# Kernel optimization log

Hardware: AMD Instinct MI355X
Metric: run time of the kernel (lower is better)

The kernel has to match this reference:

```python
import jax, jax.numpy as jnp
import numpy as np
import math

B, T, C, NH, LEVEL = 2, 2048, 1024, 16, 3


def _build_sets(T, level):
    # hierarchical dyadic sets: levels `level`..floor(log2(T)), step 2^l
    sets = []
    levelmax = int(math.floor(math.log2(T)))
    for l in range(level, levelmax + 1):
        step = 2 ** l
        for i in range(T // step):
            sets.append((i * step, (i + 1) * step - 1))
    b = np.asarray(sets, dtype=np.int32)
    return b[:, 0], b[:, 1]


def setup_inputs() -> dict:
    key = jax.random.key(0)
    kx, kw1, kw2 = jax.random.split(key, 3)
    x = jax.random.normal(kx, (B, T, C), dtype=jnp.float32)
    # torch nn.Linear stores weight as (out_features, in_features); y = x @ W.T
    W_attn = jax.random.normal(kw1, (3 * C, C), dtype=jnp.float32) * (C ** -0.5)
    W_proj = jax.random.normal(kw2, (C, C), dtype=jnp.float32) * (C ** -0.5)
    return {"x": x, "W_attn": W_attn, "W_proj": W_proj}


def _get_slice(xc, l_idx, r_idx):
    # xc: (B,NH,T,hs) cumulative sums; returns sum over [l_idx, r_idx]
    r = xc[:, :, r_idx, :]
    l = xc[:, :, l_idx - 1, :] * (l_idx >= 1)[None, None, :, None].astype(xc.dtype)
    return r - l


def _forward(x, W_attn, W_proj):
    hs = C // NH
    scale = hs ** -0.5
    qkv = x @ W_attn.T                      # (B,T,3C)
    q, k, v = jnp.split(qkv, 3, axis=2)
    heads = lambda t: t.reshape(B, T, NH, hs).transpose(0, 2, 1, 3)  # (B,NH,T,hs)
    q, k, v = heads(q), heads(k), heads(v)
    phi = lambda t: jax.nn.elu(t) + 1.0     # feature_map = 'elu_plus'
    q_phi, k_phi = phi(q), phi(k)
    k_cum = jnp.cumsum(k_phi, axis=2)
    v_cum = jnp.cumsum(v, axis=2)

    l_np, r_np = _build_sets(T, LEVEL)
    l_idx, r_idx = jnp.asarray(l_np), jnp.asarray(r_np)
    K = _get_slice(k_cum, l_idx, r_idx)     # (B,NH,S,hs)
    V = _get_slice(v_cum, l_idx, r_idx)

    t_idx = jnp.arange(T)
    mask = t_idx[:, None] >= r_idx[None, :]                 # (T,S)
    logits = jnp.einsum('bhtd,bhsd->bhts', q, K) * scale    # raw q here (as in source)
    logits = jnp.where(mask[None, None], logits, -jnp.inf)

    # tail term over last (t mod 2^level)+1 tokens, uses q_phi
    Lmin = 2 ** LEVEL
    tail_len = t_idx % Lmin + 1
    l_tail = t_idx - tail_len + 1
    K_tail = _get_slice(k_cum, l_tail, t_idx)               # (B,NH,T,hs)
    V_tail = _get_slice(v_cum, l_tail, t_idx)
    tail_logit = jnp.sum(q_phi * K_tail, axis=-1) * scale   # (B,NH,T)

    full = jnp.concatenate([logits, tail_logit[..., None]], axis=-1)
    att = jax.nn.softmax(full, axis=-1)
    out = jnp.einsum('bhts,bhsd->bhtd', att[..., :-1], V) + att[..., -1:] * V_tail
    out = out.transpose(0, 2, 1, 3).reshape(B, T, C)
    return out @ W_proj.T


def reference(x, W_attn, W_proj):
    return _forward(x, W_attn, W_proj)
```

## Files before the change

### kernel.cpp

```cpp
#include <hip/hip_runtime.h>
#include <hip/hip_bf16.h>
#include <stdint.h>

#define B_    2
#define T_    2048
#define CD    1024
#define NH_   16
#define HS_   64
#define NSETS 511
#define NSP   512
#define QKV_LD 3072
#define NEGBIG (-3.4e38f)

typedef __attribute__((ext_vector_type(8))) short  short8;
typedef __attribute__((ext_vector_type(4))) float  f32x4;

__device__ __forceinline__ unsigned short f2bf(float f) {
  unsigned u = __float_as_uint(f);
  unsigned r = 0x7FFFu + ((u >> 16) & 1u);
  return (unsigned short)((u + r) >> 16);
}
__device__ __forceinline__ float bf2f(unsigned short h) {
  return __uint_as_float(((unsigned)h) << 16);
}
__device__ __forceinline__ float elu1(float x) {
  return x > 0.f ? x + 1.f : __expf(x);
}
__device__ __forceinline__ void gload16(const unsigned short* g, short* l) {
  __builtin_amdgcn_global_load_lds(
      (const __attribute__((address_space(1))) unsigned int*)g,
      (__attribute__((address_space(3))) unsigned int*)l, 16, 0, 0);
}

__global__ __launch_bounds__(256) void split3_kernel(
    const float* __restrict__ x, const float* __restrict__ Wa,
    const float* __restrict__ Wp,
    unsigned short* __restrict__ xh, unsigned short* __restrict__ xl,
    unsigned short* __restrict__ wah, unsigned short* __restrict__ wal,
    unsigned short* __restrict__ wph) {
  int bid = blockIdx.x;
  const float* src; unsigned short *hi, *lo; int base;
  if (bid < 16384)      { src = x;  hi = xh;  lo = xl;  base = bid; }
  else if (bid < 24576) { src = Wa; hi = wah; lo = wal; base = bid - 16384; }
  else if (bid < 28672) { src = Wa; hi = wah; lo = nullptr; base = bid - 16384; }
  else                  { src = Wp; hi = wph; lo = nullptr; base = bid - 28672; }
  int i = base * 256 + threadIdx.x;
  float v = src[i];
  unsigned short h = f2bf(v);
  hi[i] = h;
  if (lo) lo[i] = f2bf(v - bf2f(h));
}

template<int SPLIT>
__device__ __forceinline__ void gemm_body(
    short* lds,
    const unsigned short* __restrict__ Ah, const unsigned short* __restrict__ Al,
    const unsigned short* __restrict__ Bh, const unsigned short* __restrict__ Bl,
    float* __restrict__ Cmat, int K, int ldc, int row0, int col0)
{
  const int tid  = threadIdx.x;
  const int lane = tid & 63;
  const int w    = tid >> 6;
  const int wr   = w >> 1, wc = w & 1;

  f32x4 acc[4][4];
  #pragma unroll
  for (int a = 0; a < 4; ++a)
    #pragma unroll
    for (int b = 0; b < 4; ++b)
      acc[a][b] = (f32x4){0.f, 0.f, 0.f, 0.f};

  const int rlane = lane & 15;
  const int kgrp  = lane >> 4;
  const int rsw   = (kgrp ^ (rlane & 3) ^ ((rlane >> 2) & 3)) << 4;

  const int slr = lane >> 2;
  const int sch = (lane & 3) ^ (slr & 3) ^ ((slr >> 2) & 3);

  const unsigned short* ssrc;
  size_t srb;
  short* sbase;
  if (SPLIT) {
    ssrc = (w == 0) ? Ah : (w == 1) ? Bh : (w == 2) ? Al : Bl;
    srb  = (w & 1) ? (size_t)col0 : (size_t)row0;
    sbase = &lds[w * 4096];
  } else {
    ssrc = (w & 1) ? Bh : Ah;
    srb  = (w & 1) ? (size_t)col0 : (size_t)row0;
    sbase = &lds[(w & 1) * 4096 + (w >> 1) * 2048];
    srb += (size_t)(w >> 1) * 64;
  }

  for (int kt = 0; kt < K; kt += 32) {
    __syncthreads();
    const unsigned short* g0 = ssrc + (srb + slr) * K + kt + (sch << 3);
    if (SPLIT) {
      #pragma unroll
      for (int i = 0; i < 8; ++i)
        gload16(g0 + (size_t)i * 16 * K, sbase + i * 512);
    } else {
      #pragma unroll
      for (int i = 0; i < 4; ++i)
        gload16(g0 + (size_t)i * 16 * K, sbase + i * 512);
    }
    __syncthreads();

    short8 aH[4], bH[4], aL[4], bL[4];
    #pragma unroll
    for (int m = 0; m < 4; ++m) {
      int r    = wr * 64 + m * 16 + rlane;
      int cidx = wc * 64 + m * 16 + rlane;
      aH[m] = *(const short8*)((const char*)lds + r * 64 + rsw);
      bH[m] = *(const short8*)((const char*)lds + 8192 + cidx * 64 + rsw);
      if (SPLIT) {
        aL[m] = *(const short8*)((const char*)lds + 16384 + r * 64 + rsw);
        bL[m] = *(const short8*)((const char*)lds + 24576 + cidx * 64 + rsw);
      }
    }
    #pragma unroll
    for (int mm = 0; mm < 4; ++mm)
      #pragma unroll
      for (int nn = 0; nn < 4; ++nn) {
        acc[mm][nn] = __builtin_amdgcn_mfma_f32_16x16x32_bf16(aH[mm], bH[nn], acc[mm][nn], 0, 0, 0);
        if (SPLIT) {
          acc[mm][nn] = __builtin_amdgcn_mfma_f32_16x16x32_bf16(aH[mm], bL[nn], acc[mm][nn], 0, 0, 0);
          acc[mm][nn] = __builtin_amdgcn_mfma_f32_16x16x32_bf16(aL[mm], bH[nn], acc[mm][nn], 0, 0, 0);
        }
      }
  }

  const int rl = (lane >> 4) * 4;
  const int cl = lane & 15;
  #pragma unroll
  for (int mm = 0; mm < 4; ++mm)
    #pragma unroll
    for (int nn = 0; nn < 4; ++nn)
      #pragma unroll
      for (int r = 0; r < 4; ++r) {
        int row = row0 + wr * 64 + mm * 16 + rl + r;
        int col = col0 + wc * 64 + nn * 16 + cl;
        Cmat[(size_t)row * ldc + col] = acc[mm][nn][r];
      }
}

__global__ __launch_bounds__(256) void gemm_qkv(
    const unsigned short* __restrict__ xh, const unsigned short* __restrict__ xl,
    const unsigned short* __restrict__ wah, const unsigned short* __restrict__ wal,
    float* __restrict__ qkv)
{
  __shared__ short lds[4 * 4096];
  int bid = blockIdx.x;
  if (bid < 512) {
    int swb = (bid & 7) * 64 + (bid >> 3);
    int bx = swb & 15, by = swb >> 4;
    gemm_body<1>(lds, xh, xl, wah, wal, qkv,
                 CD, QKV_LD, by * 128, bx * 128);
  } else {
    int p = bid - 512;
    int swb = (p & 7) * 32 + (p >> 3);
    int bx = swb & 7, by = swb >> 3;
    gemm_body<0>(lds, xh, nullptr, wah + (size_t)2048 * CD, nullptr,
                 qkv + 2048, CD, QKV_LD, by * 128, bx * 128);
  }
}

template<int SPLIT>
__global__ __launch_bounds__(256) void gemm_bt(
    const unsigned short* __restrict__ Ah, const unsigned short* __restrict__ Al,
    const unsigned short* __restrict__ Bh, const unsigned short* __restrict__ Bl,
    float* __restrict__ Cmat, int M, int N, int K, int ldc)
{
  constexpr int NT = SPLIT ? 4 : 2;
  __shared__ short lds[NT * 4096];
  const int nwg = gridDim.x;
  const int cpx = nwg >> 3;
  const int bid = blockIdx.x;
  const int swb = (bid & 7) * cpx + (bid >> 3);
  const int nbx = N >> 7;
  const int bx = swb % nbx;
  const int by = swb / nbx;
  gemm_body<SPLIT>(lds, Ah, Al, Bh, Bl, Cmat, K, ldc, by * 128, bx * 128);
}

__global__ __launch_bounds__(256) void cs_part(const float* __restrict__ qkv,
                                               float* __restrict__ part) {
  int blk = blockIdx.x;
  int q   = blk & 1;
  int seg = (blk >> 1) & 63;
  int b   = blk >> 7;
  int c   = threadIdx.x * 4;
  const float* src = qkv + (size_t)(b * T_ + seg * 32) * QKV_LD + CD + q * CD + c;
  float4 s = {0.f, 0.f, 0.f, 0.f};
  #pragma unroll 4
  for (int j = 0; j < 32; ++j) {
    float4 v = *(const float4*)(src + (size_t)j * QKV_LD);
    if (q == 0) {
      s.x += elu1(v.x); s.y += elu1(v.y); s.z += elu1(v.z); s.w += elu1(v.w);
    } else {
      s.x += v.x; s.y += v.y; s.z += v.z; s.w += v.w;
    }
  }
  *(float4*)(part + ((size_t)(b * 64 + seg) * 2048) + q * 1024 + c) = s;
}

__global__ void cs_prefix(float* __restrict__ part) {
  int idx = blockIdx.x * 256 + threadIdx.x;
  int b  = idx >> 11;
  int cc = idx & 2047;
  float v[64];
  #pragma unroll
  for (int s = 0; s < 64; ++s) v[s] = part[(size_t)(b * 64 + s) * 2048 + cc];
  float run = 0.f;
  #pragma unroll
  for (int s = 0; s < 64; ++s) { float t = v[s]; v[s] = run; run += t; }
  #pragma unroll
  for (int s = 0; s < 64; ++s) part[(size_t)(b * 64 + s) * 2048 + cc] = v[s];
}

__global__ __launch_bounds__(256) void cs_final(const float* __restrict__ qkv,
                                                const float* __restrict__ part,
                                                float* __restrict__ kcum,
                                                float* __restrict__ vcum) {
  int blk = blockIdx.x;
  int q   = blk & 1;
  int seg = (blk >> 1) & 63;
  int b   = blk >> 7;
  int c   = threadIdx.x * 4;
  int h   = c >> 6, d = c & 63;
  const float* src = qkv + (size_t)(b * T_ + seg * 32) * QKV_LD + CD + q * CD + c;
  float* dst = (q == 0 ? kcum : vcum) + ((size_t)(b * NH_ + h) * T_ + seg * 32) * HS_ + d;
  float4 s = *(const float4*)(part + ((size_t)(b * 64 + seg) * 2048) + q * 1024 + c);
  #pragma unroll 4
  for (int j = 0; j < 32; ++j) {
    float4 v = *(const float4*)(src + (size_t)j * QKV_LD);
    if (q == 0) {
      s.x += elu1(v.x); s.y += elu1(v.y); s.z += elu1(v.z); s.w += elu1(v.w);
    } else {
      s.x += v.x; s.y += v.y; s.z += v.z; s.w += v.w;
    }
    *(float4*)(dst + (size_t)j * HS_) = s;
  }
}

__global__ void build_sets(const float* __restrict__ kcum, const float* __restrict__ vcum,
                           unsigned short* __restrict__ Ksh, unsigned short* __restrict__ Ksl,
                           float* __restrict__ Vs, int* __restrict__ r_srt) {
  int idx = blockIdx.x * 256 + threadIdx.x;
  if (idx >= B_ * NH_ * NSP * HS_) return;
  int d  = idx & 63;
  int s  = (idx >> 6) & (NSP - 1);
  int bh = idx >> (6 + 9);
  if (s == NSETS) {
    size_t o = ((size_t)(bh << 9) + s) * HS_ + d;
    Ksh[o] = 0; Ksl[o] = 0; Vs[o] = 0.f;
    if (bh == 0 && d == 0) r_srt[s] = 0x7fffffff;
    return;
  }
  int lvl = 3, base = 0;
  while (s >= base + (T_ >> lvl)) { base += T_ >> lvl; ++lvl; }
  int i  = s - base;
  int m  = (i + 1) << lvl;
  int r  = m - 1;
  int li = i << lvl;
  int rank = lvl - 3;
  #pragma unroll
  for (int j = 3; j <= 11; ++j) rank += (m - 8) >> j;

  size_t rowr = ((size_t)bh * T_ + r) * HS_ + d;
  float kr = kcum[rowr], vr = vcum[rowr];
  if (li > 0) {
    size_t rowl = ((size_t)bh * T_ + li - 1) * HS_ + d;
    kr -= kcum[rowl];
    vr -= vcum[rowl];
  }
  size_t o = ((size_t)(bh << 9) + rank) * HS_ + d;
  unsigned short kh = f2bf(kr);
  Ksh[o] = kh;
  Ksl[o] = f2bf(kr - bf2f(kh));
  Vs[o]  = vr;
  if (bh == 0 && d == 0) r_srt[rank] = r;
}

__global__ __launch_bounds__(256) void vst_transpose(
    const float* __restrict__ Vs, unsigned short* __restrict__ Vst) {
  __shared__ float tile[64][65];
  int bh = blockIdx.x >> 3;
  int s0 = (blockIdx.x & 7) * 64;
  int tid = threadIdx.x;
  int srow = tid >> 2, c0 = (tid & 3) * 16;
  const float* src = Vs + ((size_t)(bh << 9) + s0 + srow) * HS_ + c0;
  #pragma unroll
  for (int j = 0; j < 4; ++j) {
    float4 v = *(const float4*)(src + j * 4);
    tile[srow][c0 + j*4 + 0] = v.x; tile[srow][c0 + j*4 + 1] = v.y;
    tile[srow][c0 + j*4 + 2] = v.z; tile[srow][c0 + j*4 + 3] = v.w;
  }
  __syncthreads();
  int d = tid >> 2, sq = (tid & 3) * 16;
  short8 a, b;
  #pragma unroll
  for (int j = 0; j < 8; ++j) {
    a[j] = (short)f2bf(tile[sq + j][d]);
    b[j] = (short)f2bf(tile[sq + 8 + j][d]);
  }
  unsigned short* dst = Vst + ((size_t)(bh << 6) + d) * NSP + s0 + sq;
  *(short8*)dst = a;
  *(short8*)(dst + 8) = b;
}

__global__ __launch_bounds__(256) void attn_mfma(
    const float* __restrict__ qkv, const float* __restrict__ kcum,
    const float* __restrict__ vcum,
    const unsigned short* __restrict__ Ksh, const unsigned short* __restrict__ Ksl,
    const unsigned short* __restrict__ Vst, const int* __restrict__ r_srt,
    unsigned short* __restrict__ attnb)
{
  __shared__ short Pl[4 * 2048];
  __shared__ short KV[3 * 4096];
  __shared__ int   rs_lds[NSP];

  const int blk = blockIdx.x;
  const int xcd = blk & 7;
  const int j   = blk >> 3;
  const int bhx = j >> 4;
  const int bh  = xcd * 4 + bhx;
  const int rb  = ((j & 15) + bhx * 4) & 15;
  const int b = bh >> 4, h = bh & 15;
  const int t0 = rb * 128;
  const int tid = threadIdx.x;
  const int lane = tid & 63;
  const int w = tid >> 6;
  const int col = lane & 15;
  const int kgrp = (lane >> 4) * 8;
  const float scale = 0.125f;

  const int srow = lane >> 3;
  const int scsw = ((lane & 7) ^ srow) * 8;

  auto stage_tile = [&](int s0) {
    #pragma unroll
    for (int L = w * 6; L < w * 6 + 6; ++L) {
      int a = L >> 3, i = L & 7;
      const unsigned short* src;
      if (a == 0)      src = Ksh + ((size_t)(bh << 9) + s0 + i * 8 + srow) * 64 + scsw;
      else if (a == 1) src = Ksl + ((size_t)(bh << 9) + s0 + i * 8 + srow) * 64 + scsw;
      else             src = Vst + ((size_t)(bh << 6) + i * 8 + srow) * NSP + s0 + scsw;
      gload16(src, KV + a * 4096 + i * 512 + lane * 8);
    }
  };

  short8 qh[2][2], ql[2][2];
  #pragma unroll
  for (int rr = 0; rr < 2; ++rr) {
    int qrow = t0 + w * 32 + rr * 16 + col;
    const float* qr = qkv + (size_t)(b * T_ + qrow) * QKV_LD + h * HS_;
    #pragma unroll
    for (int ks = 0; ks < 2; ++ks) {
      float4 v0 = *(const float4*)(qr + kgrp + ks * 32);
      float4 v1 = *(const float4*)(qr + kgrp + ks * 32 + 4);
      float vv[8] = {v0.x, v0.y, v0.z, v0.w, v1.x, v1.y, v1.z, v1.w};
      #pragma unroll
      for (int jj = 0; jj < 8; ++jj) {
        unsigned short hi = f2bf(vv[jj]);
        qh[rr][ks][jj] = (short)hi;
        ql[rr][ks][jj] = (short)f2bf(vv[jj] - bf2f(hi));
      }
    }
  }
  for (int s = tid; s < NSP; s += 256) rs_lds[s] = r_srt[s];

  int rows[2][4];
  #pragma unroll
  for (int rr = 0; rr < 2; ++rr)
    #pragma unroll
    for (int r = 0; r < 4; ++r)
      rows[rr][r] = t0 + w * 32 + rr * 16 + (lane >> 4) * 4 + r;

  f32x4 O[2][4];
  float mrun[2][4], lsum[2][4];
  #pragma unroll
  for (int rr = 0; rr < 2; ++rr)
    #pragma unroll
    for (int f = 0; f < 4; ++f) {
      O[rr][f] = (f32x4){0.f, 0.f, 0.f, 0.f};
      mrun[rr][f] = NEGBIG; lsum[rr][f] = 0.f;
    }

  int nmax = 0;
  #pragma unroll
  for (int jj = 3; jj <= 11; ++jj) nmax += (t0 + 128) >> jj;
  const int ntiles = (nmax + 63) >> 6;

  for (int tile = 0; tile < ntiles; ++tile) {
    const int s0 = tile * 64;
    stage_tile(s0);
    __syncthreads();

    f32x4 S[2][4];
    #pragma unroll
    for (int rr = 0; rr < 2; ++rr)
      #pragma unroll
      for (int f = 0; f < 4; ++f) S[rr][f] = (f32x4){0.f, 0.f, 0.f, 0.f};

    #pragma unroll
    for (int ks = 0; ks < 2; ++ks) {
      int chnk = (lane >> 4) + ks * 4;
      #pragma unroll
      for (int f = 0; f < 4; ++f) {
        int so = f * 16 + col;
        int kb = so * 128 + ((chnk ^ (so & 7)) << 4);
        short8 bHv = *(const short8*)((const char*)KV + kb);
        short8 bLv = *(const short8*)((const char*)KV + 8192 + kb);
        #pragma unroll
        for (int rr = 0; rr < 2; ++rr) {
          S[rr][f] = __builtin_amdgcn_mfma_f32_16x16x32_bf16(qh[rr][ks], bHv, S[rr][f], 0, 0, 0);
          S[rr][f] = __builtin_amdgcn_mfma_f32_16x16x32_bf16(qh[rr][ks], bLv, S[rr][f], 0, 0, 0);
          S[rr][f] = __builtin_amdgcn_mfma_f32_16x16x32_bf16(ql[rr][ks], bHv, S[rr][f], 0, 0, 0);
        }
      }
    }

    int rsv[4];
    #pragma unroll
    for (int f = 0; f < 4; ++f) rsv[f] = rs_lds[s0 + f * 16 + col];

    #pragma unroll
    for (int rr = 0; rr < 2; ++rr)
      #pragma unroll
      for (int f = 0; f < 4; ++f)
        #pragma unroll
        for (int r = 0; r < 4; ++r)
          S[rr][f][r] = (rsv[f] > rows[rr][r]) ? NEGBIG : S[rr][f][r] * scale;

    float mx[2][4];
    int pred = 1;
    #pragma unroll
    for (int rr = 0; rr < 2; ++rr)
      #pragma unroll
      for (int r = 0; r < 4; ++r) {
        mx[rr][r] = fmaxf(fmaxf(S[rr][0][r], S[rr][1][r]),
                          fmaxf(S[rr][2][r], S[rr][3][r]));
        pred &= (mx[rr][r] <= mrun[rr][r] + 8.f);
      }
    if (!__all(pred)) {
      #pragma unroll
      for (int rr = 0; rr < 2; ++rr)
        #pragma unroll
        for (int r = 0; r < 4; ++r) {
          float mt = mx[rr][r];
          mt = fmaxf(mt, __shfl_xor(mt, 1));
          mt = fmaxf(mt, __shfl_xor(mt, 2));
          mt = fmaxf(mt, __shfl_xor(mt, 4));
          mt = fmaxf(mt, __shfl_xor(mt, 8));
          float mv = fmaxf(mrun[rr][r], mt);
          float fs = __expf(mrun[rr][r] - mv);
          lsum[rr][r] *= fs;
          #pragma unroll
          for (int f = 0; f < 4; ++f) O[rr][f][r] *= fs;
          mrun[rr][r] = mv;
        }
    }

    char* pw = (char*)Pl + w * 4096;
    #pragma unroll
    for (int rr = 0; rr < 2; ++rr)
      #pragma unroll
      for (int r = 0; r < 4; ++r) {
        int rowr = rr * 16 + (lane >> 4) * 4 + r;
        int rswz = (rowr & 7) << 4;
        #pragma unroll
        for (int f = 0; f < 4; ++f) {
          float p = __expf(S[rr][f][r] - mrun[rr][r]);
          p = (rsv[f] > rows[rr][r]) ? 0.f : p;
          lsum[rr][r] += p;
          int addr = (rowr * 128 + (f * 16 + col) * 2) ^ rswz;
          *(unsigned short*)(pw + addr) = f2bf(p);
        }
      }

    #pragma unroll
    for (int ks = 0; ks < 2; ++ks) {
      int chnk = (lane >> 4) + ks * 4;
      int pb0 = (col * 128 + (kgrp + ks * 32) * 2) ^ ((col & 7) << 4);
      short8 pa0 = *(const short8*)(pw + pb0);
      short8 pa1 = *(const short8*)(pw + 2048 + pb0);
      #pragma unroll
      for (int f = 0; f < 4; ++f) {
        int dr = f * 16 + col;
        short8 bv = *(const short8*)((const char*)KV + 16384 + dr * 128 + ((chnk ^ (dr & 7)) << 4));
        O[0][f] = __builtin_amdgcn_mfma_f32_16x16x32_bf16(pa0, bv, O[0][f], 0, 0, 0);
        O[1][f] = __builtin_amdgcn_mfma_f32_16x16x32_bf16(pa1, bv, O[1][f], 0, 0, 0);
      }
    }

    __syncthreads();
  }

  float lrun[2][4];
  #pragma unroll
  for (int rr = 0; rr < 2; ++rr)
    #pragma unroll
    for (int r = 0; r < 4; ++r) {
      float l = lsum[rr][r];
      l += __shfl_xor(l, 1);
      l += __shfl_xor(l, 2);
      l += __shfl_xor(l, 4);
      l += __shfl_xor(l, 8);
      lrun[rr][r] = l;
    }

  float ztail[2];
  #pragma unroll
  for (int rr = 0; rr < 2; ++rr) {
    int trow = lane >> 2;
    int t = t0 + w * 32 + rr * 16 + trow;
    int d0 = (lane & 3) * 16;
    const float* qr = qkv + (size_t)(b * T_ + t) * QKV_LD + h * HS_ + d0;
    float qv[16];
    #pragma unroll
    for (int jj = 0; jj < 4; ++jj) {
      float4 v = *(const float4*)(qr + jj * 4);
      qv[jj*4+0] = v.x; qv[jj*4+1] = v.y; qv[jj*4+2] = v.z; qv[jj*4+3] = v.w;
    }
    int lt = t & ~7;
    const float* kc1 = kcum + ((size_t)bh * T_ + t) * HS_ + d0;
    float kt[16];
    if (lt > 0) {
      const float* kc0 = kcum + ((size_t)bh * T_ + (lt - 1)) * HS_ + d0;
      #pragma unroll
      for (int jj = 0; jj < 16; ++jj) kt[jj] = kc1[jj] - kc0[jj];
    } else {
      #pragma unroll
      for (int jj = 0; jj < 16; ++jj) kt[jj] = kc1[jj];
    }
    float z = 0.f;
    #pragma unroll
    for (int jj = 0; jj < 16; ++jj) {
      float qp = qv[jj] > 0.f ? qv[jj] + 1.f : __expf(qv[jj]);
      z += qp * kt[jj];
    }
    z += __shfl_xor(z, 1);
    z += __shfl_xor(z, 2);
    ztail[rr] = z * scale;
  }

  #pragma unroll
  for (int rr = 0; rr < 2; ++rr)
    #pragma unroll
    for (int r = 0; r < 4; ++r) {
      float zt = __shfl(ztail[rr], ((lane >> 4) * 4 + r) * 4);
      float mv = fmaxf(mrun[rr][r], zt);
      float fs = __expf(mrun[rr][r] - mv);
      float pwgt = __expf(zt - mv);
      lrun[rr][r] = lrun[rr][r] * fs + pwgt;
      int tr = rows[rr][r];
      int ltr = tr & ~7;
      #pragma unroll
      for (int f = 0; f < 4; ++f) {
        int d = f * 16 + col;
        float v1 = vcum[((size_t)bh * T_ + tr) * HS_ + d];
        float vt = (ltr > 0) ? v1 - vcum[((size_t)bh * T_ + (ltr - 1)) * HS_ + d] : v1;
        O[rr][f][r] = O[rr][f][r] * fs + pwgt * vt;
      }
    }

  #pragma unroll
  for (int rr = 0; rr < 2; ++rr)
    #pragma unroll
    for (int r = 0; r < 4; ++r) {
      float inv = 1.f / lrun[rr][r];
      unsigned short* orow = attnb + (size_t)(b * T_ + rows[rr][r]) * CD + h * HS_;
      #pragma unroll
      for (int f = 0; f < 4; ++f)
        orow[f * 16 + col] = f2bf(O[rr][f][r] * inv);
    }
}

extern "C" void kernel_launch(void* const* d_in, const int* in_sizes, int n_in,
                              void* d_out, int out_size, void* d_ws, size_t ws_size,
                              hipStream_t stream) {
  const float* x  = (const float*)d_in[0];
  const float* Wa = (const float*)d_in[1];
  const float* Wp = (const float*)d_in[2];
  float* out = (float*)d_out;

  char* ws = (char*)d_ws;
  size_t off = 0;
  auto alloc = [&](size_t bytes) -> char* {
    char* p = ws + off;
    off += (bytes + 255) & ~(size_t)255;
    return p;
  };

  const int M = B_ * T_;
  float* qkv  = (float*)alloc((size_t)M * QKV_LD * 4);
  float* kcum = (float*)alloc((size_t)B_ * NH_ * T_ * HS_ * 4);
  float* vcum = (float*)alloc((size_t)B_ * NH_ * T_ * HS_ * 4);
  float* part = (float*)alloc((size_t)B_ * 64 * 2048 * 4);
  unsigned short* wph = (unsigned short*)alloc((size_t)CD * CD * 2);

  char* regionA = alloc((size_t)16777216);
  unsigned short* xh = (unsigned short*)regionA;
  unsigned short* xl = (unsigned short*)(regionA + (size_t)M * CD * 2);
  const size_t SETS_ELEMS = (size_t)B_ * NH_ * NSP * HS_;
  unsigned short* Ksh = (unsigned short*)regionA;
  unsigned short* Ksl = Ksh + SETS_ELEMS;
  float*          Vss = (float*)(regionA + 2 * SETS_ELEMS * 2);
  unsigned short* Vst = (unsigned short*)(regionA + 2 * SETS_ELEMS * 2 + SETS_ELEMS * 4);
  int*            r_srt = (int*)(regionA + 2 * SETS_ELEMS * 2 + SETS_ELEMS * 4 + SETS_ELEMS * 2);

  char* regionB = alloc((size_t)12582912);
  unsigned short* wah = (unsigned short*)regionB;
  unsigned short* wal = (unsigned short*)(regionB + (size_t)3 * CD * CD * 2);
  unsigned short* attnb = (unsigned short*)regionB;

  split3_kernel<<<dim3(32768), dim3(256), 0, stream>>>(
      x, Wa, Wp, xh, xl, wah, wal, wph);

  gemm_qkv<<<dim3(768), dim3(256), 0, stream>>>(xh, xl, wah, wal, qkv);

  cs_part<<<dim3(B_ * 64 * 2), dim3(256), 0, stream>>>(qkv, part);
  cs_prefix<<<dim3(B_ * 2048 / 256), dim3(256), 0, stream>>>(part);
  cs_final<<<dim3(B_ * 64 * 2), dim3(256), 0, stream>>>(qkv, part, kcum, vcum);

  build_sets<<<dim3((B_ * NH_ * NSP * HS_) / 256), dim3(256), 0, stream>>>(
      kcum, vcum, Ksh, Ksl, Vss, r_srt);
  vst_transpose<<<dim3(B_ * NH_ * (NSP / 64)), dim3(256), 0, stream>>>(Vss, Vst);

  attn_mfma<<<dim3(512), dim3(256), 0, stream>>>(
      qkv, kcum, vcum, Ksh, Ksl, Vst, r_srt, attnb);

  gemm_bt<0><<<dim3((CD / 128) * (M / 128)), dim3(256), 0, stream>>>(
      attnb, (const unsigned short*)nullptr, wph, (const unsigned short*)nullptr,
      out, M, CD, CD, CD);
}
```

Before: 227.0 us.

## Double-buffer attention tiles, fuse set building, drop prefix kernel, split QKV GEMM

The attention kernel now double-buffers its K/V LDS tiles, issuing the next tile's global loads before computing on the current one, which removes one barrier per iteration. build_sets and vst_transpose are fused into one kernel that writes bf16 transposed V directly, so the fp32 intermediate is gone. The cs_prefix kernel is removed and each cs_final block sums the preceding partials itself. The combined QKV GEMM launch is split into two gemm_bt launches. This cuts launches and memory traffic at the cost of more LDS in attention and redundant prefix reads in cs_final.

Result: no change. 230.1 us (+1.4%).

```diff
diff --git a/kernel.cpp b/kernel.cpp
--- a/kernel.cpp
+++ b/kernel.cpp
@@ -143,27 +143,6 @@
       }
 }
 
-__global__ __launch_bounds__(256) void gemm_qkv(
-    const unsigned short* __restrict__ xh, const unsigned short* __restrict__ xl,
-    const unsigned short* __restrict__ wah, const unsigned short* __restrict__ wal,
-    float* __restrict__ qkv)
-{
-  __shared__ short lds[4 * 4096];
-  int bid = blockIdx.x;
-  if (bid < 512) {
-    int swb = (bid & 7) * 64 + (bid >> 3);
-    int bx = swb & 15, by = swb >> 4;
-    gemm_body<1>(lds, xh, xl, wah, wal, qkv,
-                 CD, QKV_LD, by * 128, bx * 128);
-  } else {
-    int p = bid - 512;
-    int swb = (p & 7) * 32 + (p >> 3);
-    int bx = swb & 7, by = swb >> 3;
-    gemm_body<0>(lds, xh, nullptr, wah + (size_t)2048 * CD, nullptr,
-                 qkv + 2048, CD, QKV_LD, by * 128, bx * 128);
-  }
-}
-
 template<int SPLIT>
 __global__ __launch_bounds__(256) void gemm_bt(
     const unsigned short* __restrict__ Ah, const unsigned short* __restrict__ Al,
@@ -203,20 +182,6 @@
   *(float4*)(part + ((size_t)(b * 64 + seg) * 2048) + q * 1024 + c) = s;
 }
 
-__global__ void cs_prefix(float* __restrict__ part) {
-  int idx = blockIdx.x * 256 + threadIdx.x;
-  int b  = idx >> 11;
-  int cc = idx & 2047;
-  float v[64];
-  #pragma unroll
-  for (int s = 0; s < 64; ++s) v[s] = part[(size_t)(b * 64 + s) * 2048 + cc];
-  float run = 0.f;
-  #pragma unroll
-  for (int s = 0; s < 64; ++s) { float t = v[s]; v[s] = run; run += t; }
-  #pragma unroll
-  for (int s = 0; s < 64; ++s) part[(size_t)(b * 64 + s) * 2048 + cc] = v[s];
-}
-
 __global__ __launch_bounds__(256) void cs_final(const float* __restrict__ qkv,
                                                 const float* __restrict__ part,
                                                 float* __restrict__ kcum,
@@ -227,9 +192,15 @@
   int b   = blk >> 7;
   int c   = threadIdx.x * 4;
   int h   = c >> 6, d = c & 63;
+  float4 s = {0.f, 0.f, 0.f, 0.f};
+  const float* pb = part + (size_t)(b * 64) * 2048 + q * 1024 + c;
+  #pragma unroll 8
+  for (int ss = 0; ss < seg; ++ss) {
+    float4 p = *(const float4*)(pb + (size_t)ss * 2048);
+    s.x += p.x; s.y += p.y; s.z += p.z; s.w += p.w;
+  }
   const float* src = qkv + (size_t)(b * T_ + seg * 32) * QKV_LD + CD + q * CD + c;
   float* dst = (q == 0 ? kcum : vcum) + ((size_t)(b * NH_ + h) * T_ + seg * 32) * HS_ + d;
-  float4 s = *(const float4*)(part + ((size_t)(b * 64 + seg) * 2048) + q * 1024 + c);
   #pragma unroll 4
   for (int j = 0; j < 32; ++j) {
     float4 v = *(const float4*)(src + (size_t)j * QKV_LD);
@@ -242,70 +213,93 @@
   }
 }
 
-__global__ void build_sets(const float* __restrict__ kcum, const float* __restrict__ vcum,
-                           unsigned short* __restrict__ Ksh, unsigned short* __restrict__ Ksl,
-                           float* __restrict__ Vs, int* __restrict__ r_srt) {
-  int idx = blockIdx.x * 256 + threadIdx.x;
-  if (idx >= B_ * NH_ * NSP * HS_) return;
-  int d  = idx & 63;
-  int s  = (idx >> 6) & (NSP - 1);
-  int bh = idx >> (6 + 9);
-  if (s == NSETS) {
-    size_t o = ((size_t)(bh << 9) + s) * HS_ + d;
-    Ksh[o] = 0; Ksl[o] = 0; Vs[o] = 0.f;
-    if (bh == 0 && d == 0) r_srt[s] = 0x7fffffff;
-    return;
-  }
-  int lvl = 3, base = 0;
-  while (s >= base + (T_ >> lvl)) { base += T_ >> lvl; ++lvl; }
-  int i  = s - base;
-  int m  = (i + 1) << lvl;
-  int r  = m - 1;
-  int li = i << lvl;
-  int rank = lvl - 3;
-  #pragma unroll
-  for (int j = 3; j <= 11; ++j) rank += (m - 8) >> j;
-
-  size_t rowr = ((size_t)bh * T_ + r) * HS_ + d;
-  float kr = kcum[rowr], vr = vcum[rowr];
-  if (li > 0) {
-    size_t rowl = ((size_t)bh * T_ + li - 1) * HS_ + d;
-    kr -= kcum[rowl];
-    vr -= vcum[rowl];
-  }
-  size_t o = ((size_t)(bh << 9) + rank) * HS_ + d;
-  unsigned short kh = f2bf(kr);
-  Ksh[o] = kh;
-  Ksl[o] = f2bf(kr - bf2f(kh));
-  Vs[o]  = vr;
-  if (bh == 0 && d == 0) r_srt[rank] = r;
-}
-
-__global__ __launch_bounds__(256) void vst_transpose(
-    const float* __restrict__ Vs, unsigned short* __restrict__ Vst) {
-  __shared__ float tile[64][65];
-  int bh = blockIdx.x >> 3;
-  int s0 = (blockIdx.x & 7) * 64;
-  int tid = threadIdx.x;
-  int srow = tid >> 2, c0 = (tid & 3) * 16;
-  const float* src = Vs + ((size_t)(bh << 9) + s0 + srow) * HS_ + c0;
-  #pragma unroll
-  for (int j = 0; j < 4; ++j) {
-    float4 v = *(const float4*)(src + j * 4);
-    tile[srow][c0 + j*4 + 0] = v.x; tile[srow][c0 + j*4 + 1] = v.y;
-    tile[srow][c0 + j*4 + 2] = v.z; tile[srow][c0 + j*4 + 3] = v.w;
+__global__ __launch_bounds__(256) void build_sets2(
+    const float* __restrict__ kcum, const float* __restrict__ vcum,
+    unsigned short* __restrict__ Ksh, unsigned short* __restrict__ Ksl,
+    unsigned short* __restrict__ Vst, int* __restrict__ r_srt)
+{
+  __shared__ int   lr[64], lli[64];
+  __shared__ float vt[64][65];
+  const int bh = blockIdx.x >> 3;
+  const int s0 = (blockIdx.x & 7) * 64;
+  const int tid = threadIdx.x;
+
+  for (int s = tid; s < NSP; s += 256) {
+    int r, li, rank;
+    if (s == NSETS) { r = 0x7fffffff; li = 0; rank = NSETS; }
+    else {
+      int lvl = 3, base = 0;
+      while (s >= base + (T_ >> lvl)) { base += T_ >> lvl; ++lvl; }
+      int i = s - base;
+      int m = (i + 1) << lvl;
+      r = m - 1; li = i << lvl;
+      rank = lvl - 3;
+      #pragma unroll
+      for (int j = 3; j <= 11; ++j) rank += (m - 8) >> j;
+    }
+    if (rank >= s0 && rank < s0 + 64) {
+      lr[rank - s0]  = r;
+      lli[rank - s0] = li;
+      if (bh == 0) r_srt[rank] = r;
+    }
   }
   __syncthreads();
-  int d = tid >> 2, sq = (tid & 3) * 16;
-  short8 a, b;
+
+  const int sl = tid >> 2;
+  const int dq = (tid & 3) * 16;
+  const int r  = lr[sl], li = lli[sl];
+  const size_t orow = ((size_t)(bh << 9) + s0 + sl) * HS_ + dq;
+  short8 kh0, kh1, kl0, kl1;
+  if (r == 0x7fffffff) {
+    #pragma unroll
+    for (int j = 0; j < 8; ++j) { kh0[j]=0; kh1[j]=0; kl0[j]=0; kl1[j]=0; }
+    #pragma unroll
+    for (int j = 0; j < 16; ++j) vt[sl][dq + j] = 0.f;
+  } else {
+    const float* kr0 = kcum + ((size_t)bh * T_ + r) * HS_ + dq;
+    const float* vr0 = vcum + ((size_t)bh * T_ + r) * HS_ + dq;
+    const float* kr1 = kcum + ((size_t)bh * T_ + (li - 1)) * HS_ + dq;
+    const float* vr1 = vcum + ((size_t)bh * T_ + (li - 1)) * HS_ + dq;
+    #pragma unroll
+    for (int g = 0; g < 4; ++g) {
+      float4 kv = *(const float4*)(kr0 + g * 4);
+      float4 vv = *(const float4*)(vr0 + g * 4);
+      if (li > 0) {
+        float4 k1 = *(const float4*)(kr1 + g * 4);
+        float4 v1 = *(const float4*)(vr1 + g * 4);
+        kv.x -= k1.x; kv.y -= k1.y; kv.z -= k1.z; kv.w -= k1.w;
+        vv.x -= v1.x; vv.y -= v1.y; vv.z -= v1.z; vv.w -= v1.w;
+      }
+      float ka[4] = {kv.x, kv.y, kv.z, kv.w};
+      float va[4] = {vv.x, vv.y, vv.z, vv.w};
+      #pragma unroll
+      for (int j = 0; j < 4; ++j) {
+        int e = g * 4 + j;
+        unsigned short h = f2bf(ka[j]);
+        unsigned short l = f2bf(ka[j] - bf2f(h));
+        if (e < 8) { kh0[e] = (short)h; kl0[e] = (short)l; }
+        else       { kh1[e - 8] = (short)h; kl1[e - 8] = (short)l; }
+        vt[sl][dq + e] = va[j];
+      }
+    }
+  }
+  *(short8*)(Ksh + orow)     = kh0;
+  *(short8*)(Ksh + orow + 8) = kh1;
+  *(short8*)(Ksl + orow)     = kl0;
+  *(short8*)(Ksl + orow + 8) = kl1;
+  __syncthreads();
+
+  const int d  = tid >> 2;
+  const int sq = (tid & 3) * 16;
+  short8 a, b2;
   #pragma unroll
   for (int j = 0; j < 8; ++j) {
-    a[j] = (short)f2bf(tile[sq + j][d]);
-    b[j] = (short)f2bf(tile[sq + 8 + j][d]);
+    a[j]  = (short)f2bf(vt[sq + j][d]);
+    b2[j] = (short)f2bf(vt[sq + 8 + j][d]);
   }
   unsigned short* dst = Vst + ((size_t)(bh << 6) + d) * NSP + s0 + sq;
   *(short8*)dst = a;
-  *(short8*)(dst + 8) = b;
+  *(short8*)(dst + 8) = b2;
 }
 
 __global__ __launch_bounds__(256) void attn_mfma(
@@ -316,7 +310,7 @@
     unsigned short* __restrict__ attnb)
 {
   __shared__ short Pl[4 * 2048];
-  __shared__ short KV[3 * 4096];
+  __shared__ short KV[2][3 * 4096];
   __shared__ int   rs_lds[NSP];
 
   const int blk = blockIdx.x;
@@ -337,7 +331,7 @@
   const int srow = lane >> 3;
   const int scsw = ((lane & 7) ^ srow) * 8;
 
-  auto stage_tile = [&](int s0) {
+  auto stage_tile = [&](short* kv, int s0) {
     #pragma unroll
     for (int L = w * 6; L < w * 6 + 6; ++L) {
       int a = L >> 3, i = L & 7;
@@ -345,7 +339,7 @@
       if (a == 0)      src = Ksh + ((size_t)(bh << 9) + s0 + i * 8 + srow) * 64 + scsw;
       else if (a == 1) src = Ksl + ((size_t)(bh << 9) + s0 + i * 8 + srow) * 64 + scsw;
       else             src = Vst + ((size_t)(bh << 6) + i * 8 + srow) * NSP + s0 + scsw;
-      gload16(src, KV + a * 4096 + i * 512 + lane * 8);
+      gload16(src, kv + a * 4096 + i * 512 + lane * 8);
     }
   };
 
@@ -368,6 +362,8 @@
     }
   }
   for (int s = tid; s < NSP; s += 256) rs_lds[s] = r_srt[s];
+  stage_tile(&KV[0][0], 0);
+  __syncthreads();
 
   int rows[2][4];
   #pragma unroll
@@ -390,12 +386,13 @@
   #pragma unroll
   for (int jj = 3; jj <= 11; ++jj) nmax += (t0 + 128) >> jj;
   const int ntiles = (nmax + 63) >> 6;
+  int cur = 0;
 
   for (int tile = 0; tile < ntiles; ++tile) {
     const int s0 = tile * 64;
-    stage_tile(s0);
-    __syncthreads();
-
+    if (tile + 1 < ntiles) stage_tile(&KV[cur ^ 1][0], s0 + 64);
+
+    const char* kc = (const char*)&KV[cur][0];
     f32x4 S[2][4];
     #pragma unroll
     for (int rr = 0; rr < 2; ++rr)
@@ -409,8 +406,8 @@
       for (int f = 0; f < 4; ++f) {
         int so = f * 16 + col;
         int kb = so * 128 + ((chnk ^ (so & 7)) << 4);
-        short8 bHv = *(const short8*)((const char*)KV + kb);
-        short8 bLv = *(const short8*)((const char*)KV + 8192 + kb);
+        short8 bHv = *(const short8*)(kc + kb);
+        short8 bLv = *(const short8*)(kc + 8192 + kb);
         #pragma unroll
         for (int rr = 0; rr < 2; ++rr) {
           S[rr][f] = __builtin_amdgcn_mfma_f32_16x16x32_bf16(qh[rr][ks], bHv, S[rr][f], 0, 0, 0);
@@ -487,13 +484,14 @@
       #pragma unroll
       for (int f = 0; f < 4; ++f) {
         int dr = f * 16 + col;
-        short8 bv = *(const short8*)((const char*)KV + 16384 + dr * 128 + ((chnk ^ (dr & 7)) << 4));
+        short8 bv = *(const short8*)(kc + 16384 + dr * 128 + ((chnk ^ (dr & 7)) << 4));
         O[0][f] = __builtin_amdgcn_mfma_f32_16x16x32_bf16(pa0, bv, O[0][f], 0, 0, 0);
         O[1][f] = __builtin_amdgcn_mfma_f32_16x16x32_bf16(pa1, bv, O[1][f], 0, 0, 0);
       }
     }
 
     __syncthreads();
+    cur ^= 1;
   }
 
   float lrun[2][4];
@@ -605,9 +603,8 @@
   const size_t SETS_ELEMS = (size_t)B_ * NH_ * NSP * HS_;
   unsigned short* Ksh = (unsigned short*)regionA;
   unsigned short* Ksl = Ksh + SETS_ELEMS;
-  float*          Vss = (float*)(regionA + 2 * SETS_ELEMS * 2);
-  unsigned short* Vst = (unsigned short*)(regionA + 2 * SETS_ELEMS * 2 + SETS_ELEMS * 4);
-  int*            r_srt = (int*)(regionA + 2 * SETS_ELEMS * 2 + SETS_ELEMS * 4 + SETS_ELEMS * 2);
+  unsigned short* Vst = (unsigned short*)(regionA + 2 * SETS_ELEMS * 2);
+  int*            r_srt = (int*)(regionA + 3 * SETS_ELEMS * 2);
 
   char* regionB = alloc((size_t)12582912);
   unsigned short* wah = (unsigned short*)regionB;
@@ -617,15 +614,18 @@
   split3_kernel<<<dim3(32768), dim3(256), 0, stream>>>(
       x, Wa, Wp, xh, xl, wah, wal, wph);
 
-  gemm_qkv<<<dim3(768), dim3(256), 0, stream>>>(xh, xl, wah, wal, qkv);
+  gemm_bt<1><<<dim3((2048 / 128) * (M / 128)), dim3(256), 0, stream>>>(
+      xh, xl, wah, wal, qkv, M, 2048, CD, QKV_LD);
+
+  gemm_bt<0><<<dim3((1024 / 128) * (M / 128)), dim3(256), 0, stream>>>(
+      xh, (const unsigned short*)nullptr, wah + (size_t)2048 * CD,
+      (const unsigned short*)nullptr, qkv + 2048, M, 1024, CD, QKV_LD);
 
   cs_part<<<dim3(B_ * 64 * 2), dim3(256), 0, stream>>>(qkv, part);
-  cs_prefix<<<dim3(B_ * 2048 / 256), dim3(256), 0, stream>>>(part);
   cs_final<<<dim3(B_ * 64 * 2), dim3(256), 0, stream>>>(qkv, part, kcum, vcum);
 
-  build_sets<<<dim3((B_ * NH_ * NSP * HS_) / 256), dim3(256), 0, stream>>>(
-      kcum, vcum, Ksh, Ksl, Vss, r_srt);
-  vst_transpose<<<dim3(B_ * NH_ * (NSP / 64)), dim3(256), 0, stream>>>(Vss, Vst);
+  build_sets2<<<dim3(B_ * NH_ * 8), dim3(256), 0, stream>>>(
+      kcum, vcum, Ksh, Ksl, Vst, r_srt);
 
   attn_mfma<<<dim3(512), dim3(256), 0, stream>>>(
       qkv, kcum, vcum, Ksh, Ksl, Vst, r_srt, attnb);
```
